# Optimization experiments

Measured on AMD Instinct MI355X. Metric: run time of the kernel, lower is better.

## Reference

```python
import jax, jax.numpy as jnp
import numpy as np

B, T, E = 2, 2048, 1024
H = 16
D = E // H  # head_dim = 64


def setup_inputs() -> dict:
    key = jax.random.key(0)
    ks = jax.random.split(key, 9)
    s = 1.0 / np.sqrt(E)
    inp = {"x": jax.random.normal(ks[0], (B, T, E), dtype=jnp.float32)}
    # Linear params (torch nn.Linear: y = x @ W.T + b)
    inp["Wq"] = jax.random.uniform(ks[1], (E, E), jnp.float32, -s, s)
    inp["bq"] = jax.random.uniform(ks[2], (E,), jnp.float32, -s, s)
    inp["Wk"] = jax.random.uniform(ks[3], (E, E), jnp.float32, -s, s)
    inp["bk"] = jax.random.uniform(ks[4], (E,), jnp.float32, -s, s)
    inp["Wv"] = jax.random.uniform(ks[5], (E, E), jnp.float32, -s, s)
    inp["bv"] = jax.random.uniform(ks[6], (E,), jnp.float32, -s, s)
    inp["Wo"] = jax.random.uniform(ks[7], (E, E), jnp.float32, -s, s)
    inp["bo"] = jax.random.uniform(ks[8], (E,), jnp.float32, -s, s)
    return inp


def reference(x, Wq, bq, Wk, bk, Wv, bv, Wo, bo):
    # QKV projections, reshape to [B, H, T, D]
    def split_heads(y):
        return y.reshape(B, T, H, D).transpose(0, 2, 1, 3)

    Q = split_heads(x @ Wq.T + bq)
    K = split_heads(x @ Wk.T + bk)
    V = split_heads(x @ Wv.T + bv)

    scale = 1.0 / jnp.sqrt(jnp.asarray(D, x.dtype))
    scores = jnp.einsum("bhqd,bhkd->bhqk", Q, K) * scale  # [B,H,T,T]
    attn = jax.nn.softmax(scores, axis=-1)
    out = jnp.einsum("bhqk,bhkd->bhqd", attn, V)  # [B,H,T,D]
    out = out.transpose(0, 2, 1, 3).reshape(B, T, E)
    # dropout is identity in eval mode
    return out @ Wo.T + bo
```

## Files before the change

kernel.cpp:

```cpp
#include <hip/hip_runtime.h>
#include <math.h>

#define BB 2
#define TT 2048
#define EE 1024
#define HH 16
#define DD 64
#define MM (BB*TT)
#define KK EE

typedef short bf16x8 __attribute__((ext_vector_type(8)));
typedef float f32x4  __attribute__((ext_vector_type(4)));
typedef float f32x16 __attribute__((ext_vector_type(16)));
typedef unsigned int u32x4 __attribute__((ext_vector_type(4)));

__device__ __forceinline__ unsigned short f2bf(float f) {
  unsigned int u = __float_as_uint(f);
  u = (u + 0x7FFFu + ((u >> 16) & 1u)) >> 16;
  return (unsigned short)u;
}

__device__ __forceinline__ unsigned int cvtpk(float lo, float hi) {
  unsigned int r;
  asm("v_cvt_pk_bf16_f32 %0, %1, %2" : "=v"(r) : "v"(lo), "v"(hi));
  return r;
}

__device__ __forceinline__ void plswap(unsigned int &a, unsigned int &b) {
  asm("v_permlane32_swap_b32 %0, %1" : "+v"(a), "+v"(b));
}

__device__ __forceinline__ void async16(const void* g, void* l) {
  __builtin_amdgcn_global_load_lds(
      (const __attribute__((address_space(1))) unsigned int*)g,
      (__attribute__((address_space(3))) unsigned int*)l, 16, 0, 0);
}

__global__ __launch_bounds__(256) void to_bf16(
    const float* __restrict__ x,  const float* __restrict__ wq,
    const float* __restrict__ wk, const float* __restrict__ wv,
    const float* __restrict__ wo,
    unsigned short* __restrict__ xh, unsigned short* __restrict__ wcat,
    unsigned short* __restrict__ woh)
{
  int c = blockIdx.x * 256 + threadIdx.x;
  const float* src; unsigned short* dst; int off;
  if (c < 1048576) { src = x; dst = xh; off = c; }
  else {
    int r = c - 1048576;
    int w = r >> 18;
    off = r & 262143;
    if      (w == 0) { src = wq; dst = wcat; }
    else if (w == 1) { src = wk; dst = wcat + (1 << 20); }
    else if (w == 2) { src = wv; dst = wcat + (2 << 20); }
    else             { src = wo; dst = woh; }
  }
  float4 v = ((const float4*)src)[off];
  ushort4 h;
  h.x = f2bf(v.x); h.y = f2bf(v.y); h.z = f2bf(v.z); h.w = f2bf(v.w);
  ((ushort4*)dst)[off] = h;
}

template<int MODE>
__global__ __launch_bounds__(512) void gemm_bf16(
    const unsigned short* __restrict__ A, const unsigned short* __restrict__ B,
    const float* __restrict__ b0p, const float* __restrict__ b1p,
    const float* __restrict__ b2p,
    unsigned short* __restrict__ oq, unsigned short* __restrict__ ok,
    unsigned short* __restrict__ ov, float* __restrict__ ofp, float qscale)
{
  constexpr int NT = (MODE == 0) ? 128 : 64;
  constexpr int JN = NT / 32;
  constexpr int BROWS = NT * 32;
  constexpr int TOT = (MODE == 0) ? 16 : 12;
  __shared__ unsigned short S[(MODE == 0) ? 17408 : 12288];

  const int tid  = threadIdx.x;
  const int lane = tid & 63;
  const int wv   = tid >> 6;
  const int col  = lane & 15;
  const int quad = lane >> 4;
  const int wm = (wv & 3) * 32;
  const int wn = (wv >> 2) * (NT / 2);
  const int m0 = blockIdx.x * 128;
  const int n0 = blockIdx.y * NT;

  const int srow = lane >> 2;
  const int sw16 = (((lane & 3) ^ ((lane >> 2) & 3)) << 3);
  const int fswA = ((quad ^ (col & 3)) << 3);

  auto stage = [&](int kt, int b) {
#pragma unroll
    for (int s = 0; s < 2; ++s) {
      const int t = wv * 2 + s;
      if (t < TOT) {
        const unsigned short* src; int rb, g0, loff;
        if (t < 8) { src = A; rb = t * 16;       g0 = m0; loff = b * 4096; }
        else       { src = B; rb = (t - 8) * 16; g0 = n0; loff = 8192 + b * BROWS; }
        async16(src + (size_t)(g0 + rb + srow) * KK + kt + sw16,
                S + loff + rb * 32);
      }
    }
  };

  f32x4 acc[2][JN];
  const f32x4 z = {0.f, 0.f, 0.f, 0.f};
#pragma unroll
  for (int i = 0; i < 2; ++i)
#pragma unroll
    for (int j = 0; j < JN; ++j) acc[i][j] = z;

  stage(0, 0);
  __syncthreads();

  for (int kt = 0; kt < KK; kt += 32) {
    const int buf = (kt >> 5) & 1;
    if (kt + 32 < KK) stage(kt + 32, buf ^ 1);

    const unsigned short* Asb = S + buf * 4096;
    const unsigned short* Bsb = S + 8192 + buf * BROWS;
    bf16x8 bf[JN];
#pragma unroll
    for (int j = 0; j < JN; ++j)
      bf[j] = *(const bf16x8*)(Bsb + (wn + j * 16 + col) * 32 + fswA);
#pragma unroll
    for (int i = 0; i < 2; ++i) {
      bf16x8 af = *(const bf16x8*)(Asb + (wm + i * 16 + col) * 32 + fswA);
#pragma unroll
      for (int j = 0; j < JN; ++j)
        acc[i][j] = __builtin_amdgcn_mfma_f32_16x16x32_bf16(af, bf[j], acc[i][j], 0, 0, 0);
    }
    __syncthreads();
  }

  unsigned short* Cs = S;
  if (MODE == 0) {
    const int region = n0 >> 10;
    const float* bias = (region == 0) ? b0p : (region == 1) ? b1p : b2p;
    const float scl = (region == 0) ? qscale : 1.0f;
    const int nlbase = n0 & 1023;
    const int h0 = nlbase >> 6;
    const int b = m0 >> 11, t0 = m0 & (TT - 1);
    if (region < 2) {
#pragma unroll
      for (int i = 0; i < 2; ++i)
#pragma unroll
        for (int j = 0; j < 4; ++j) {
          const int nt = wn + j * 16 + col;
          const float bs = bias[nlbase + nt];
#pragma unroll
          for (int r = 0; r < 4; ++r) {
            const int mt = wm + i * 16 + quad * 4 + r;
            Cs[mt * 136 + nt] = f2bf((acc[i][j][r] + bs) * scl);
          }
        }
      __syncthreads();
      unsigned short* dst = (region == 0) ? oq : ok;
#pragma unroll
      for (int s = 0; s < 4; ++s) {
        const int u = s * 512 + tid;
        const int mt = u >> 4, hs = (u >> 3) & 1, ch = u & 7;
        const size_t g = ((size_t)(b * HH + h0 + hs) * TT + t0 + mt) * DD + ch * 8;
        *(uint4*)(dst + g) = *(const uint4*)(Cs + mt * 136 + hs * 64 + ch * 8);
      }
    } else {
#pragma unroll
      for (int i = 0; i < 2; ++i)
#pragma unroll
        for (int j = 0; j < 4; ++j) {
          const int nt = wn + j * 16 + col;
          const float bs = bias[nlbase + nt];
          ushort4 pk;
          pk.x = f2bf(acc[i][j][0] + bs);
          pk.y = f2bf(acc[i][j][1] + bs);
          pk.z = f2bf(acc[i][j][2] + bs);
          pk.w = f2bf(acc[i][j][3] + bs);
          *(ushort4*)(Cs + nt * 136 + wm + i * 16 + quad * 4) = pk;
        }
      __syncthreads();
#pragma unroll
      for (int s = 0; s < 4; ++s) {
        const int u = s * 512 + tid;
        const int nt = u >> 4, ch = u & 15;
        const int d = nt & 63, hs = nt >> 6;
        const size_t g = ((size_t)(b * HH + h0 + hs) * DD + d) * TT + t0 + ch * 8;
        *(uint4*)(ov + g) = *(const uint4*)(Cs + nt * 136 + ch * 8);
      }
    }
  } else {
#pragma unroll
    for (int i = 0; i < 2; ++i) {
#pragma unroll
      for (int j = 0; j < JN; ++j) {
        const int n = n0 + wn + j * 16 + col;
        const float bs = b0p[n];
#pragma unroll
        for (int r = 0; r < 4; ++r) {
          const int m = m0 + wm + i * 16 + quad * 4 + r;
          ofp[(size_t)m * EE + n] = acc[i][j][r] + bs;
        }
      }
    }
  }
}

__global__ __launch_bounds__(512, 4) void flash_mfma(
    const unsigned short* __restrict__ Qb, const unsigned short* __restrict__ Kb,
    const unsigned short* __restrict__ Vtb, unsigned short* __restrict__ ctx)
{
  __shared__ unsigned short Qs[128 * 64];
  __shared__ unsigned short Ks[4][64 * 64];
  __shared__ unsigned short Vts[4][64 * 64];

  const int tid  = threadIdx.x;
  const int lane = tid & 63;
  const int wv   = tid >> 6;
  const int lq   = lane & 31;
  const int hf   = lane >> 5;
  const int wq   = wv & 3;
  const int wk2  = wv >> 2;
  const int gid  = blockIdx.x;
  const int bh   = gid & 31;
  const int q0   = (gid >> 5) * 128;

  const unsigned short* Qg = Qb  + (size_t)bh * TT * DD;
  const unsigned short* Kg = Kb  + (size_t)bh * TT * DD;
  const unsigned short* Vg = Vtb + (size_t)bh * DD * TT;

  const int srow = lane >> 3;
  const int sw16 = (((lane & 7) ^ ((lane >> 3) & 7)) << 3);

  const int rbK = wq * 16;
  const bool isK = (wv < 4);
  const unsigned short* g0 =
      (isK ? Kg + (size_t)(rbK + srow) * DD : Vg + (size_t)(rbK + srow) * TT) + sw16;
  const unsigned short* g1 = g0 + (isK ? 8 * DD : 8 * TT);
  unsigned short* l0 = (isK ? &Ks[0][0] : &Vts[0][0]) + rbK * 64;
  unsigned short* l1 = l0 + 8 * 64;
  const int gstep = isK ? 64 * DD : 64;

  auto stage_kv = [&](int ti, int slot) {
    const size_t go = (size_t)ti * gstep;
    async16(g0 + go, l0 + slot * 4096);
    async16(g1 + go, l1 + slot * 4096);
  };

  int koff[4], voff[2][2];
#pragma unroll
  for (int s = 0; s < 4; ++s)
    koff[s] = ((wk2 * 32 + lq) * 64 + (((2 * s + hf) ^ (lane & 7)) << 3)) * 2;
#pragma unroll
  for (int m = 0; m < 2; ++m)
#pragma unroll
    for (int sg = 0; sg < 2; ++sg)
      voff[m][sg] = ((m * 32 + lq) * 64 +
                     (((wk2 * 4 + 2 * sg + hf) ^ (lane & 7)) << 3)) * 2;

#pragma unroll
  for (int s = 0; s < 2; ++s) {
    const int rb = wv * 16 + s * 8;
    async16(Qg + (size_t)(q0 + rb + srow) * DD + sw16, &Qs[rb * 64]);
  }
  stage_kv(0, 0);
  stage_kv(1, 1);
  __syncthreads();

  bf16x8 aq[4];
#pragma unroll
  for (int s = 0; s < 4; ++s)
    aq[s] = *(const bf16x8*)(Qs + (wq * 32 + lq) * 64 +
                             (((2 * s + hf) ^ (lane & 7)) << 3));

  const f32x16 z16 = {0.f,0.f,0.f,0.f,0.f,0.f,0.f,0.f,
                      0.f,0.f,0.f,0.f,0.f,0.f,0.f,0.f};
  f32x16 o_acc[2], sacc, nsacc;
  o_acc[0] = z16; o_acc[1] = z16;
  float lpart = 0.f;

  {
    const char* Kp = (const char*)&Ks[0][0];
    sacc = z16;
#pragma unroll
    for (int s = 0; s < 4; ++s) {
      bf16x8 ak = *(const bf16x8*)(Kp + koff[s]);
      sacc = __builtin_amdgcn_mfma_f32_32x32x16_bf16(ak, aq[s], sacc, 0, 0, 0);
    }
  }

#define BODY(T, S0, S1, S2, DOSTAGE, DOQK, VMC, SIN, SOUT) do {               \
    if (DOSTAGE) stage_kv((T) + 2, S2);                                       \
    asm volatile("s_waitcnt vmcnt(" #VMC ")" ::: "memory");                   \
    __builtin_amdgcn_sched_barrier(0);                                        \
    __builtin_amdgcn_s_barrier();                                             \
    __builtin_amdgcn_sched_barrier(0);                                        \
    bf16x8 pa0, pa1;                                                          \
    {      \
      float e0 = __builtin_amdgcn_exp2f(SIN[0]);                              \
      float e1 = __builtin_amdgcn_exp2f(SIN[1]);                              \
      float e2 = __builtin_amdgcn_exp2f(SIN[2]);                              \
      float e3 = __builtin_amdgcn_exp2f(SIN[3]);                              \
      float e4 = __builtin_amdgcn_exp2f(SIN[4]);                              \
      float e5 = __builtin_amdgcn_exp2f(SIN[5]);                              \
      float e6 = __builtin_amdgcn_exp2f(SIN[6]);                              \
      float e7 = __builtin_amdgcn_exp2f(SIN[7]);                              \
      lpart += ((e0 + e1) + (e2 + e3)) + ((e4 + e5) + (e6 + e7));             \
      unsigned int a0 = cvtpk(e0, e1), b0 = cvtpk(e4, e5);                    \
      unsigned int a1 = cvtpk(e2, e3), b1 = cvtpk(e6, e7);                    \
      plswap(a0, b0); plswap(a1, b1);                                         \
      u32x4 w = {a0, a1, b0, b1};                                             \
      pa0 = __builtin_bit_cast(bf16x8, w);                                    \
    }                                                                         \
    {                                                     \
      float e0 = __builtin_amdgcn_exp2f(SIN[8]);                              \
      float e1 = __builtin_amdgcn_exp2f(SIN[9]);                              \
      float e2 = __builtin_amdgcn_exp2f(SIN[10]);                             \
      float e3 = __builtin_amdgcn_exp2f(SIN[11]);                             \
      float e4 = __builtin_amdgcn_exp2f(SIN[12]);                             \
      float e5 = __builtin_amdgcn_exp2f(SIN[13]);                             \
      float e6 = __builtin_amdgcn_exp2f(SIN[14]);                             \
      float e7 = __builtin_amdgcn_exp2f(SIN[15]);                             \
      lpart += ((e0 + e1) + (e2 + e3)) + ((e4 + e5) + (e6 + e7));             \
      unsigned int a0 = cvtpk(e0, e1), b0 = cvtpk(e4, e5);                    \
      unsigned int a1 = cvtpk(e2, e3), b1 = cvtpk(e6, e7);                    \
      plswap(a0, b0); plswap(a1, b1);                                         \
      u32x4 w = {a0, a1, b0, b1};                                             \
      pa1 = __builtin_bit_cast(bf16x8, w);                                    \
    }                                                                         \
    __builtin_amdgcn_s_setprio(1);                                            \
    if (DOQK) {                      \
      const char* Kp = (const char*)&Ks[S1][0];                               \
      f32x16 ns = z16;                                                        \
      _Pragma("unroll")                                                       \
      for (int s = 0; s < 4; ++s) {                                           \
        bf16x8 ak = *(const bf16x8*)(Kp + koff[s]);                           \
        ns = __builtin_amdgcn_mfma_f32_32x32x16_bf16(ak, aq[s], ns, 0, 0, 0); \
      }                                                                       \
      SOUT = ns;                                                              \
    }                                                                         \
    {                                                              \
      const char* Vp = (const char*)&Vts[S0][0];                              \
      _Pragma("unroll")                                                       \
      for (int m = 0; m < 2; ++m) {                                           \
        bf16x8 v0 = *(const bf16x8*)(Vp + voff[m][0]);                        \
        bf16x8 v1 = *(const bf16x8*)(Vp + voff[m][1]);                        \
        o_acc[m] = __builtin_amdgcn_mfma_f32_32x32x16_bf16(pa0, v0, o_acc[m], 0, 0, 0); \
        o_acc[m] = __builtin_amdgcn_mfma_f32_32x32x16_bf16(pa1, v1, o_acc[m], 0, 0, 0); \
      }                                                                       \
    }                                                                         \
    __builtin_amdgcn_s_setprio(0);                                            \
  } while (0)

  for (int t = 0; t < 28; t += 4) {
    BODY(t + 0, 0, 1, 2, 1, 1, 2, sacc, nsacc);
    BODY(t + 1, 1, 2, 3, 1, 1, 2, nsacc, sacc);
    BODY(t + 2, 2, 3, 0, 1, 1, 2, sacc, nsacc);
    BODY(t + 3, 3, 0, 1, 1, 1, 2, nsacc, sacc);
  }
  BODY(28, 0, 1, 2, 1, 1, 2, sacc, nsacc);
  BODY(29, 1, 2, 3, 1, 1, 2, nsacc, sacc);
  BODY(30, 2, 3, 0, 0, 1, 0, sacc, nsacc);
  BODY(31, 3, 0, 1, 0, 0, 0, nsacc, sacc);
#undef BODY

  float* Qf = (float*)&Qs[0];
  float* Of = (float*)&Ks[0][0];
  unsigned short* Cs = &Vts[0][0];
  const int bq = bh >> 4, head = bh & 15;

  float lw = lpart + __shfl_xor(lpart, 32);
  if (lane < 32) Qf[wv * 32 + lane] = lw;
  __syncthreads();

  if (wv >= 4) {
#pragma unroll
    for (int m = 0; m < 2; ++m)
#pragma unroll
      for (int r = 0; r < 16; ++r) {
        const int ql = (r & 3) + 8 * (r >> 2) + 4 * hf;
        Of[wq * 2048 + ql * 64 + m * 32 + lq] = o_acc[m][r];
      }
  }
  __syncthreads();

  if (wv < 4) {
    float linv[16];
#pragma unroll
    for (int r = 0; r < 16; ++r) {
      const int ql = (r & 3) + 8 * (r >> 2) + 4 * hf;
      linv[r] = 1.0f / (Qf[wv * 32 + ql] + Qf[(wv + 4) * 32 + ql]);
    }
#pragma unroll
    for (int m = 0; m < 2; ++m)
#pragma unroll
      for (int r = 0; r < 16; ++r) {
        const int ql = (r & 3) + 8 * (r >> 2) + 4 * hf;
        const float val =
            (o_acc[m][r] + Of[wq * 2048 + ql * 64 + m * 32 + lq]) * linv[r];
        const int row = wq * 32 + ql, d = m * 32 + lq;
        Cs[row * 64 + (((d >> 3) ^ (row & 7)) << 3) + (d & 7)] = f2bf(val);
      }
  }
  __syncthreads();

#pragma unroll
  for (int s = 0; s < 2; ++s) {
    const int u = s * 512 + tid;
    const int mr = u >> 3, ch = u & 7;
    const size_t g = ((size_t)(bq * TT + q0 + mr)) * EE + head * DD + ch * 8;
    const int chs = (ch ^ (mr & 7)) << 3;
    *(uint4*)(ctx + g) = *(const uint4*)(Cs + mr * 64 + chs);
  }
}

extern "C" void kernel_launch(void* const* d_in, const int* in_sizes, int n_in,
                              void* d_out, int out_size, void* d_ws, size_t ws_size,
                              hipStream_t stream) {
  const float* x  = (const float*)d_in[0];
  const float* Wq = (const float*)d_in[1];
  const float* bq = (const float*)d_in[2];
  const float* Wk = (const float*)d_in[3];
  const float* bk = (const float*)d_in[4];
  const float* Wv = (const float*)d_in[5];
  const float* bv = (const float*)d_in[6];
  const float* Wo = (const float*)d_in[7];
  const float* bo = (const float*)d_in[8];

  unsigned short* p = (unsigned short*)d_ws;
  const size_t XN = (size_t)MM * EE;
  const size_t WN = (size_t)EE * EE;
  unsigned short* x_h    = p;           p += XN;
  unsigned short* Wcat_h = p;           p += 3 * WN;
  unsigned short* Wo_h   = p;           p += WN;
  unsigned short* Qb     = p;           p += XN;
  unsigned short* Kb     = p;           p += XN;
  unsigned short* Vtb    = p;           p += XN;
  unsigned short* ctx_h  = x_h;

  to_bf16<<<8192, 256, 0, stream>>>(x, Wq, Wk, Wv, Wo, x_h, Wcat_h, Wo_h);

  const float qscale = 0.125f * 1.44269504088896f;

  gemm_bf16<0><<<dim3(MM / 128, 3 * EE / 128), 512, 0, stream>>>(
      x_h, Wcat_h, bq, bk, bv, Qb, Kb, Vtb, nullptr, qscale);

  flash_mfma<<<dim3((TT / 128) * BB * HH), 512, 0, stream>>>(Qb, Kb, Vtb, ctx_h);

  gemm_bf16<2><<<dim3(MM / 128, EE / 64), 512, 0, stream>>>(
      ctx_h, Wo_h, bo, nullptr, nullptr,
      nullptr, nullptr, nullptr, (float*)d_out, 1.0f);
}
```

Measured before the change: 192.1 us.

## Use 4-slot LDS ring with prefetch depth 2 in projection GEMM

The bf16 GEMM main loop moves from double buffering with two __syncthreads per k-step to a 4-slot shared-memory ring with prefetch distance 2. Each step uses an explicit vmcnt wait and a single s_barrier, fully unrolled through a macro. This aims to hide global-load latency and drop one barrier per iteration, at the cost of more LDS per block, which may reduce occupancy. Separately, the attention QK MFMA chains now start from a zero accumulator and write directly into the destination register, removing a separate zero-init and copy.

New measurement: 190.9 us. About the same (-0.6%).

```diff
diff --git a/kernel.cpp b/kernel.cpp
--- a/kernel.cpp
+++ b/kernel.cpp
@@ -73,7 +73,7 @@
   constexpr int JN = NT / 32;
   constexpr int BROWS = NT * 32;
   constexpr int TOT = (MODE == 0) ? 16 : 12;
-  __shared__ unsigned short S[(MODE == 0) ? 17408 : 12288];
+  __shared__ unsigned short S[16384 + 4 * BROWS];
 
   const int tid  = threadIdx.x;
   const int lane = tid & 63;
@@ -89,14 +89,14 @@
   const int sw16 = (((lane & 3) ^ ((lane >> 2) & 3)) << 3);
   const int fswA = ((quad ^ (col & 3)) << 3);
 
-  auto stage = [&](int kt, int b) {
+  auto stage = [&](int kt, int slot) {
 #pragma unroll
     for (int s = 0; s < 2; ++s) {
       const int t = wv * 2 + s;
       if (t < TOT) {
         const unsigned short* src; int rb, g0, loff;
-        if (t < 8) { src = A; rb = t * 16;       g0 = m0; loff = b * 4096; }
-        else       { src = B; rb = (t - 8) * 16; g0 = n0; loff = 8192 + b * BROWS; }
+        if (t < 8) { src = A; rb = t * 16;       g0 = m0; loff = slot * 4096; }
+        else       { src = B; rb = (t - 8) * 16; g0 = n0; loff = 16384 + slot * BROWS; }
         async16(src + (size_t)(g0 + rb + srow) * KK + kt + sw16,
                 S + loff + rb * 32);
       }
@@ -111,30 +111,44 @@
     for (int j = 0; j < JN; ++j) acc[i][j] = z;
 
   stage(0, 0);
-  __syncthreads();
-
-  for (int kt = 0; kt < KK; kt += 32) {
-    const int buf = (kt >> 5) & 1;
-    if (kt + 32 < KK) stage(kt + 32, buf ^ 1);
-
-    const unsigned short* Asb = S + buf * 4096;
-    const unsigned short* Bsb = S + 8192 + buf * BROWS;
-    bf16x8 bf[JN];
-#pragma unroll
-    for (int j = 0; j < JN; ++j)
-      bf[j] = *(const bf16x8*)(Bsb + (wn + j * 16 + col) * 32 + fswA);
-#pragma unroll
-    for (int i = 0; i < 2; ++i) {
-      bf16x8 af = *(const bf16x8*)(Asb + (wm + i * 16 + col) * 32 + fswA);
-#pragma unroll
-      for (int j = 0; j < JN; ++j)
-        acc[i][j] = __builtin_amdgcn_mfma_f32_16x16x32_bf16(af, bf[j], acc[i][j], 0, 0, 0);
-    }
-    __syncthreads();
-  }
+  stage(32, 1);
+
+#define GBODY(T, SL, S2, DOSTAGE, VMC) do {                                   \
+    if (DOSTAGE) stage(((T) + 2) * 32, S2);                                   \
+    asm volatile("s_waitcnt vmcnt(" #VMC ")" ::: "memory");                   \
+    __builtin_amdgcn_sched_barrier(0);                                        \
+    __builtin_amdgcn_s_barrier();                                             \
+    __builtin_amdgcn_sched_barrier(0);                                        \
+    const unsigned short* Asb = S + (SL) * 4096;                              \
+    const unsigned short* Bsb = S + 16384 + (SL) * BROWS;                     \
+    bf16x8 bfr[JN];                                                           \
+    _Pragma("unroll")                                                         \
+    for (int j = 0; j < JN; ++j)                                              \
+      bfr[j] = *(const bf16x8*)(Bsb + (wn + j * 16 + col) * 32 + fswA);       \
+    _Pragma("unroll")                                                         \
+    for (int i = 0; i < 2; ++i) {                                             \
+      bf16x8 af = *(const bf16x8*)(Asb + (wm + i * 16 + col) * 32 + fswA);    \
+      _Pragma("unroll")                                                       \
+      for (int j = 0; j < JN; ++j)                                            \
+        acc[i][j] = __builtin_amdgcn_mfma_f32_16x16x32_bf16(af, bfr[j], acc[i][j], 0, 0, 0); \
+    }                                                                         \
+  } while (0)
+
+  for (int t = 0; t < 28; t += 4) {
+    GBODY(t + 0, 0, 2, 1, 4);
+    GBODY(t + 1, 1, 3, 1, 4);
+    GBODY(t + 2, 2, 0, 1, 4);
+    GBODY(t + 3, 3, 1, 1, 4);
+  }
+  GBODY(28, 0, 2, 1, 4);
+  GBODY(29, 1, 3, 1, 4);
+  GBODY(30, 2, 0, 0, 2);
+  GBODY(31, 3, 0, 0, 0);
+#undef GBODY
 
   unsigned short* Cs = S;
   if (MODE == 0) {
+    __syncthreads();
     const int region = n0 >> 10;
     const float* bias = (region == 0) ? b0p : (region == 1) ? b1p : b2p;
     const float scl = (region == 0) ? qscale : 1.0f;
@@ -279,10 +293,11 @@
 
   {
     const char* Kp = (const char*)&Ks[0][0];
-    sacc = z16;
-#pragma unroll
-    for (int s = 0; s < 4; ++s) {
-      bf16x8 ak = *(const bf16x8*)(Kp + koff[s]);
+    bf16x8 ak = *(const bf16x8*)(Kp + koff[0]);
+    sacc = __builtin_amdgcn_mfma_f32_32x32x16_bf16(ak, aq[0], z16, 0, 0, 0);
+#pragma unroll
+    for (int s = 1; s < 4; ++s) {
+      ak = *(const bf16x8*)(Kp + koff[s]);
       sacc = __builtin_amdgcn_mfma_f32_32x32x16_bf16(ak, aq[s], sacc, 0, 0, 0);
     }
   }
@@ -327,15 +342,15 @@
       pa1 = __builtin_bit_cast(bf16x8, w);                                    \
     }                                                                         \
     __builtin_amdgcn_s_setprio(1);                                            \
-    if (DOQK) {                      \
+    if (DOQK) {     \
       const char* Kp = (const char*)&Ks[S1][0];                               \
-      f32x16 ns = z16;                                                        \
+      bf16x8 ak = *(const bf16x8*)(Kp + koff[0]);                             \
+      SOUT = __builtin_amdgcn_mfma_f32_32x32x16_bf16(ak, aq[0], z16, 0, 0, 0);\
       _Pragma("unroll")                                                       \
-      for (int s = 0; s < 4; ++s) {                                           \
-        bf16x8 ak = *(const bf16x8*)(Kp + koff[s]);                           \
-        ns = __builtin_amdgcn_mfma_f32_32x32x16_bf16(ak, aq[s], ns, 0, 0, 0); \
+      for (int s = 1; s < 4; ++s) {                                           \
+        ak = *(const bf16x8*)(Kp + koff[s]);                                  \
+        SOUT = __builtin_amdgcn_mfma_f32_32x32x16_bf16(ak, aq[s], SOUT, 0, 0, 0); \
       }                                                                       \
-      SOUT = ns;                                                              \
     }                                                                         \
     {                                                              \
       const char* Vp = (const char*)&Vts[S0][0];                              \
```
